# Kernel tuning notes

Hardware: AMD Instinct MI355X
Metric: run time of the kernel (lower is better)

Reference implementation:

```python
import jax, jax.numpy as jnp
import numpy as np

WIN = 9
PAD = WIN // 2
WIN_SIZE = float(WIN * WIN)
EPS = 1e-5


def _box_sum(x):
    # Equivalent to conv2d with a [1,1,9,9] ones kernel, stride 1, padding 4.
    # reduce_window with add is the efficient/clean jax form of a box filter.
    return jax.lax.reduce_window(
        x, 0.0, jax.lax.add,
        window_dimensions=(1, 1, WIN, WIN),
        window_strides=(1, 1, 1, 1),
        padding=[(0, 0), (0, 0), (PAD, PAD), (PAD, PAD)],
    )


def setup_inputs() -> dict:
    key = jax.random.key(0)
    k1, k2 = jax.random.split(key)
    shape = (16, 1, 512, 512)  # [B, C=1, H, W]
    y_true = jax.random.uniform(k1, shape, dtype=jnp.float32)
    y_pred = jax.random.uniform(k2, shape, dtype=jnp.float32)
    return {"y_true": y_true, "y_pred": y_pred}


def reference(y_true, y_pred):
    Ii, Ji = y_true, y_pred

    I_sum = _box_sum(Ii)
    J_sum = _box_sum(Ji)
    I2_sum = _box_sum(Ii * Ii)
    J2_sum = _box_sum(Ji * Ji)
    IJ_sum = _box_sum(Ii * Ji)

    u_I = I_sum / WIN_SIZE
    u_J = J_sum / WIN_SIZE

    cross = IJ_sum - u_J * I_sum - u_I * J_sum + u_I * u_J * WIN_SIZE
    cross = jnp.maximum(cross, EPS)
    I_var = I2_sum - 2.0 * u_I * I_sum + u_I * u_I * WIN_SIZE
    I_var = jnp.maximum(I_var, EPS)
    J_var = J2_sum - 2.0 * u_J * J_sum + u_J * u_J * WIN_SIZE
    J_var = jnp.maximum(J_var, EPS)

    cc = (cross * cross) / (I_var * J_var)
    return -jnp.mean(cc)
```

## Files before the change

kernel.cpp:

```cpp
#include <hip/hip_runtime.h>

#define IMG    512
#define BAND   4
#define NBLK   512
#define NPIX   (16.0 * 512.0 * 512.0)
#define EPS    1e-5f
#define INV81  (1.0f / 81.0f)

struct Rows { float4 i0, i1, j0, j1; };

__device__ __forceinline__ Rows load_rows(const float* __restrict__ Ib,
                                          const float* __restrict__ Jb,
                                          int y, int col0)
{
    Rows r;
    if (y >= 0 && y < IMG) {
        const float* rI = Ib + (size_t)y * IMG + col0;
        const float* rJ = Jb + (size_t)y * IMG + col0;
        r.i0 = *(const float4*)(rI);
        r.i1 = *(const float4*)(rI + 4);
        r.j0 = *(const float4*)(rJ);
        r.j1 = *(const float4*)(rJ + 4);
    } else {
        r.i0 = r.i1 = r.j0 = r.j1 = float4{0.f, 0.f, 0.f, 0.f};
    }
    return r;
}

#define ACC(c, xv, yv)                          \
    sI[c]  += (xv); sJ[c] += (yv);              \
    sII[c]  = fmaf((xv), (xv), sII[c]);         \
    sJJ[c]  = fmaf((yv), (yv), sJJ[c]);         \
    sIJ[c]  = fmaf((xv), (yv), sIJ[c]);

#define UPD(c, nx, ny, ox, oy)                                  \
    sI[c]  += (nx) - (ox);                                      \
    sJ[c]  += (ny) - (oy);                                      \
    sII[c]  = fmaf((nx), (nx), fmaf(-(ox), (ox), sII[c]));      \
    sJJ[c]  = fmaf((ny), (ny), fmaf(-(oy), (oy), sJJ[c]));      \
    sIJ[c]  = fmaf((nx), (ny), fmaf(-(ox), (oy), sIJ[c]));

#define ACC_ROWS(R)                              \
    ACC(0, R.i0.x, R.j0.x) ACC(1, R.i0.y, R.j0.y)\
    ACC(2, R.i0.z, R.j0.z) ACC(3, R.i0.w, R.j0.w)\
    ACC(4, R.i1.x, R.j1.x) ACC(5, R.i1.y, R.j1.y)\
    ACC(6, R.i1.z, R.j1.z) ACC(7, R.i1.w, R.j1.w)

#define UPD_ROWS(NR, OR)                                                  \
    UPD(0, NR.i0.x, NR.j0.x, OR.i0.x, OR.j0.x)                            \
    UPD(1, NR.i0.y, NR.j0.y, OR.i0.y, OR.j0.y)                            \
    UPD(2, NR.i0.z, NR.j0.z, OR.i0.z, OR.j0.z)                            \
    UPD(3, NR.i0.w, NR.j0.w, OR.i0.w, OR.j0.w)                            \
    UPD(4, NR.i1.x, NR.j1.x, OR.i1.x, OR.j1.x)                            \
    UPD(5, NR.i1.y, NR.j1.y, OR.i1.y, OR.j1.y)                            \
    UPD(6, NR.i1.z, NR.j1.z, OR.i1.z, OR.j1.z)                            \
    UPD(7, NR.i1.w, NR.j1.w, OR.i1.w, OR.j1.w)

__device__ __forceinline__ void hwin(const float s[8], int lane, float w[8])
{
    float l[4], r[4];
    #pragma unroll
    for (int i = 0; i < 4; ++i) {
        float lv = __shfl_up(s[4 + i], 1, 64);
        float rv = __shfl_down(s[i],   1, 64);
        l[i] = (lane == 0)  ? 0.f : lv;
        r[i] = (lane == 63) ? 0.f : rv;
    }
    w[0] = ((l[0] + l[1]) + (l[2] + l[3])) +
           ((s[0] + s[1]) + (s[2] + s[3])) + s[4];
    w[1] = w[0] + s[5] - l[0];
    w[2] = w[1] + s[6] - l[1];
    w[3] = w[2] + s[7] - l[2];
    w[4] = w[3] + r[0] - l[3];
    w[5] = w[4] + r[1] - s[0];
    w[6] = w[5] + r[2] - s[1];
    w[7] = w[6] + r[3] - s[2];
}

__global__ __launch_bounds__(256) void ncc_band_kernel(
    const float* __restrict__ I, const float* __restrict__ J,
    double* __restrict__ slots)
{
    const int lane = threadIdx.x & 63;
    const int wid  = threadIdx.x >> 6;
    const int sblk = (blockIdx.x & 7) * (NBLK / 8) + (blockIdx.x >> 3);
    const int band = sblk * 4 + wid;
    const int img  = band >> 7;
    const int y0   = (band & 127) * BAND;
    const int col0 = lane * 8;

    const float* Ib = I + (size_t)img * IMG * IMG;
    const float* Jb = J + (size_t)img * IMG * IMG;

    float sI[8], sJ[8], sII[8], sJJ[8], sIJ[8];
    #pragma unroll
    for (int c = 0; c < 8; ++c) { sI[c]=0.f; sJ[c]=0.f; sII[c]=0.f; sJJ[c]=0.f; sIJ[c]=0.f; }

    Rows od0 = load_rows(Ib, Jb, y0 - 4, col0);
    Rows od1 = load_rows(Ib, Jb, y0 - 3, col0);
    Rows A   = load_rows(Ib, Jb, y0 - 2, col0);
    Rows B   = load_rows(Ib, Jb, y0 - 1, col0);

    ACC_ROWS(od0)
    ACC_ROWS(od1)
    ACC_ROWS(A)  A = load_rows(Ib, Jb, y0 + 0, col0);
    ACC_ROWS(B)  B = load_rows(Ib, Jb, y0 + 1, col0);
    ACC_ROWS(A)  A = load_rows(Ib, Jb, y0 + 2, col0);
    ACC_ROWS(B)  B = load_rows(Ib, Jb, y0 + 3, col0);
    ACC_ROWS(A)  A = load_rows(Ib, Jb, y0 + 4, col0);
    ACC_ROWS(B)  B = load_rows(Ib, Jb, y0 + 5, col0);
    ACC_ROWS(A)  A = load_rows(Ib, Jb, y0 + 6, col0);

    float local = 0.0f;

    auto hpass = [&]() {
        float wI[8], wJ[8], t[8], cross[8];
        hwin(sI, lane, wI);
        hwin(sJ, lane, wJ);
        hwin(sIJ, lane, t);
        #pragma unroll
        for (int k = 0; k < 8; ++k)
            cross[k] = fmaxf(fmaf(-wI[k] * INV81, wJ[k], t[k]), EPS);
        hwin(sII, lane, t);
        #pragma unroll
        for (int k = 0; k < 8; ++k)
            wI[k] = fmaxf(fmaf(-wI[k] * INV81, wI[k], t[k]), EPS);
        hwin(sJJ, lane, t);
        #pragma unroll
        for (int k = 0; k < 8; ++k)
            wJ[k] = fmaxf(fmaf(-wJ[k] * INV81, wJ[k], t[k]), EPS);
        #pragma unroll
        for (int k = 0; k < 8; ++k)
            local += (cross[k] * cross[k]) * __builtin_amdgcn_rcpf(wI[k] * wJ[k]);
    };

    hpass();
    UPD_ROWS(B, od0)
    B = load_rows(Ib, Jb, y0 + 7, col0);
    hpass();
    UPD_ROWS(A, od1)
    A = load_rows(Ib, Jb, y0 - 2, col0);
    hpass();
    UPD_ROWS(B, A)
    hpass();

    #pragma unroll
    for (int off = 32; off > 0; off >>= 1)
        local += __shfl_down(local, off, 64);

    __shared__ float wpart[4];
    if (lane == 0) wpart[wid] = local;
    __syncthreads();
    if (threadIdx.x == 0) {
        double bsum = ((double)wpart[0] + (double)wpart[1]) +
                      ((double)wpart[2] + (double)wpart[3]);
        slots[blockIdx.x] = bsum;
    }
}

__global__ __launch_bounds__(256) void ncc_finalize_kernel(
    const double* __restrict__ slots, float* __restrict__ out)
{
    const int tid = threadIdx.x;
    double2 v = *(const double2*)(slots + 2 * tid);
    double t = v.x + v.y;
    #pragma unroll
    for (int off = 32; off > 0; off >>= 1)
        t += __shfl_down(t, off, 64);

    __shared__ double wsumd[4];
    if ((tid & 63) == 0) wsumd[tid >> 6] = t;
    __syncthreads();
    if (tid == 0)
        out[0] = (float)(-((wsumd[0] + wsumd[1]) +
                           (wsumd[2] + wsumd[3])) / NPIX);
}

extern "C" void kernel_launch(void* const* d_in, const int* in_sizes, int n_in,
                              void* d_out, int out_size, void* d_ws, size_t ws_size,
                              hipStream_t stream)
{
    const float* I = (const float*)d_in[0];
    const float* J = (const float*)d_in[1];
    float* out = (float*)d_out;
    double* slots = (double*)d_ws;

    ncc_band_kernel<<<NBLK, 256, 0, stream>>>(I, J, slots);
    ncc_finalize_kernel<<<1, 256, 0, stream>>>(slots, out);
}
```

Baseline: 16.16 us.

## Split each image row across two waves with LDS edge exchange

Each band of 4 rows is now processed by two waves, each covering half the 512 columns with 4 columns per lane instead of 8. Grid size doubles to 1024 blocks. The column-sums at the seam between the two halves are exchanged through double-buffered shared memory, with a __syncthreads before each horizontal pass. The finalize kernel now reads twice as many slots. The aim is more parallelism and lower per-thread register pressure, at the cost of block-wide barriers, LDS traffic, and row loads that are 16 bytes wide instead of 32.

New measurement: 28.02 us. 1.73x slower.

```diff
diff --git a/kernel.cpp b/kernel.cpp
--- a/kernel.cpp
+++ b/kernel.cpp
@@ -2,12 +2,12 @@
 
 #define IMG    512
 #define BAND   4
-#define NBLK   512
+#define NBLK   1024
 #define NPIX   (16.0 * 512.0 * 512.0)
 #define EPS    1e-5f
 #define INV81  (1.0f / 81.0f)
 
-struct Rows { float4 i0, i1, j0, j1; };
+struct Rows { float4 i0, j0; };
 
 __device__ __forceinline__ Rows load_rows(const float* __restrict__ Ib,
                                           const float* __restrict__ Jb,
@@ -15,14 +15,11 @@
 {
     Rows r;
     if (y >= 0 && y < IMG) {
-        const float* rI = Ib + (size_t)y * IMG + col0;
-        const float* rJ = Jb + (size_t)y * IMG + col0;
-        r.i0 = *(const float4*)(rI);
-        r.i1 = *(const float4*)(rI + 4);
-        r.j0 = *(const float4*)(rJ);
-        r.j1 = *(const float4*)(rJ + 4);
+        r.i0 = *(const float4*)(Ib + (size_t)y * IMG + col0);
+        r.j0 = *(const float4*)(Jb + (size_t)y * IMG + col0);
     } else {
-        r.i0 = r.i1 = r.j0 = r.j1 = float4{0.f, 0.f, 0.f, 0.f};
+        r.i0 = float4{0.f, 0.f, 0.f, 0.f};
+        r.j0 = float4{0.f, 0.f, 0.f, 0.f};
     }
     return r;
 }
@@ -40,109 +37,137 @@
     sJJ[c]  = fmaf((ny), (ny), fmaf(-(oy), (oy), sJJ[c]));      \
     sIJ[c]  = fmaf((nx), (ny), fmaf(-(ox), (oy), sIJ[c]));
 
-#define ACC_ROWS(R)                              \
+#define ACC4(R)                                  \
     ACC(0, R.i0.x, R.j0.x) ACC(1, R.i0.y, R.j0.y)\
-    ACC(2, R.i0.z, R.j0.z) ACC(3, R.i0.w, R.j0.w)\
-    ACC(4, R.i1.x, R.j1.x) ACC(5, R.i1.y, R.j1.y)\
-    ACC(6, R.i1.z, R.j1.z) ACC(7, R.i1.w, R.j1.w)
-
-#define UPD_ROWS(NR, OR)                                                  \
+    ACC(2, R.i0.z, R.j0.z) ACC(3, R.i0.w, R.j0.w)
+
+#define UPD4(NR, OR)                                                      \
     UPD(0, NR.i0.x, NR.j0.x, OR.i0.x, OR.j0.x)                            \
     UPD(1, NR.i0.y, NR.j0.y, OR.i0.y, OR.j0.y)                            \
     UPD(2, NR.i0.z, NR.j0.z, OR.i0.z, OR.j0.z)                            \
-    UPD(3, NR.i0.w, NR.j0.w, OR.i0.w, OR.j0.w)                            \
-    UPD(4, NR.i1.x, NR.j1.x, OR.i1.x, OR.j1.x)                            \
-    UPD(5, NR.i1.y, NR.j1.y, OR.i1.y, OR.j1.y)                            \
-    UPD(6, NR.i1.z, NR.j1.z, OR.i1.z, OR.j1.z)                            \
-    UPD(7, NR.i1.w, NR.j1.w, OR.i1.w, OR.j1.w)
-
-__device__ __forceinline__ void hwin(const float s[8], int lane, float w[8])
+    UPD(3, NR.i0.w, NR.j0.w, OR.i0.w, OR.j0.w)
+
+__device__ __forceinline__ void hwin4(const float s[4], const float* lSrc,
+                                      const float* rSrc, int lane, float w[4])
 {
     float l[4], r[4];
     #pragma unroll
     for (int i = 0; i < 4; ++i) {
-        float lv = __shfl_up(s[4 + i], 1, 64);
-        float rv = __shfl_down(s[i],   1, 64);
-        l[i] = (lane == 0)  ? 0.f : lv;
-        r[i] = (lane == 63) ? 0.f : rv;
+        float lv = __shfl_up(s[i], 1, 64);
+        float rv = __shfl_down(s[i], 1, 64);
+        l[i] = (lane == 0)  ? lSrc[i] : lv;
+        r[i] = (lane == 63) ? rSrc[i] : rv;
     }
     w[0] = ((l[0] + l[1]) + (l[2] + l[3])) +
-           ((s[0] + s[1]) + (s[2] + s[3])) + s[4];
-    w[1] = w[0] + s[5] - l[0];
-    w[2] = w[1] + s[6] - l[1];
-    w[3] = w[2] + s[7] - l[2];
-    w[4] = w[3] + r[0] - l[3];
-    w[5] = w[4] + r[1] - s[0];
-    w[6] = w[5] + r[2] - s[1];
-    w[7] = w[6] + r[3] - s[2];
+           ((s[0] + s[1]) + (s[2] + s[3])) + r[0];
+    w[1] = w[0] + r[1] - l[0];
+    w[2] = w[1] + r[2] - l[1];
+    w[3] = w[2] + r[3] - l[2];
 }
 
 __global__ __launch_bounds__(256) void ncc_band_kernel(
     const float* __restrict__ I, const float* __restrict__ J,
     double* __restrict__ slots)
 {
-    const int lane = threadIdx.x & 63;
-    const int wid  = threadIdx.x >> 6;
-    const int sblk = (blockIdx.x & 7) * (NBLK / 8) + (blockIdx.x >> 3);
-    const int band = sblk * 4 + wid;
-    const int img  = band >> 7;
-    const int y0   = (band & 127) * BAND;
-    const int col0 = lane * 8;
+    const int lane  = threadIdx.x & 63;
+    const int wid   = threadIdx.x >> 6;
+    const int sblk  = (blockIdx.x & 7) * (NBLK / 8) + (blockIdx.x >> 3);
+    const int band  = sblk * 2 + (wid >> 1);
+    const int cside = wid & 1;
+    const int img   = band >> 7;
+    const int y0    = (band & 127) * BAND;
+    const int col0  = cside * 256 + lane * 4;
 
     const float* Ib = I + (size_t)img * IMG * IMG;
     const float* Jb = J + (size_t)img * IMG * IMG;
 
-    float sI[8], sJ[8], sII[8], sJJ[8], sIJ[8];
-    #pragma unroll
-    for (int c = 0; c < 8; ++c) { sI[c]=0.f; sJ[c]=0.f; sII[c]=0.f; sJJ[c]=0.f; sIJ[c]=0.f; }
+    __shared__ float eL[2][4][20];
+    __shared__ float eR[2][4][20];
+    if (threadIdx.x < 160) {
+        (&eL[0][0][0])[threadIdx.x] = 0.f;
+        (&eR[0][0][0])[threadIdx.x] = 0.f;
+    }
+    __syncthreads();
+
+    float sI[4], sJ[4], sII[4], sJJ[4], sIJ[4];
+    #pragma unroll
+    for (int c = 0; c < 4; ++c) { sI[c]=0.f; sJ[c]=0.f; sII[c]=0.f; sJJ[c]=0.f; sIJ[c]=0.f; }
 
     Rows od0 = load_rows(Ib, Jb, y0 - 4, col0);
     Rows od1 = load_rows(Ib, Jb, y0 - 3, col0);
     Rows A   = load_rows(Ib, Jb, y0 - 2, col0);
     Rows B   = load_rows(Ib, Jb, y0 - 1, col0);
 
-    ACC_ROWS(od0)
-    ACC_ROWS(od1)
-    ACC_ROWS(A)  A = load_rows(Ib, Jb, y0 + 0, col0);
-    ACC_ROWS(B)  B = load_rows(Ib, Jb, y0 + 1, col0);
-    ACC_ROWS(A)  A = load_rows(Ib, Jb, y0 + 2, col0);
-    ACC_ROWS(B)  B = load_rows(Ib, Jb, y0 + 3, col0);
-    ACC_ROWS(A)  A = load_rows(Ib, Jb, y0 + 4, col0);
-    ACC_ROWS(B)  B = load_rows(Ib, Jb, y0 + 5, col0);
-    ACC_ROWS(A)  A = load_rows(Ib, Jb, y0 + 6, col0);
+    ACC4(od0)
+    ACC4(od1)
+    ACC4(A)  A = load_rows(Ib, Jb, y0 + 0, col0);
+    ACC4(B)  B = load_rows(Ib, Jb, y0 + 1, col0);
+    ACC4(A)  A = load_rows(Ib, Jb, y0 + 2, col0);
+    ACC4(B)  B = load_rows(Ib, Jb, y0 + 3, col0);
+    ACC4(A)  A = load_rows(Ib, Jb, y0 + 4, col0);
+    ACC4(B)  B = load_rows(Ib, Jb, y0 + 5, col0);
+    ACC4(A)  A = load_rows(Ib, Jb, y0 + 6, col0);
 
     float local = 0.0f;
 
-    auto hpass = [&]() {
-        float wI[8], wJ[8], t[8], cross[8];
-        hwin(sI, lane, wI);
-        hwin(sJ, lane, wJ);
-        hwin(sIJ, lane, t);
-        #pragma unroll
-        for (int k = 0; k < 8; ++k)
+    auto edge_write = [&](int buf) {
+        if (cside == 0) {
+            if (lane == 63) {
+                float* d = &eL[buf][wid + 1][0];
+                *(float4*)(d +  0) = float4{sI[0],  sI[1],  sI[2],  sI[3]};
+                *(float4*)(d +  4) = float4{sJ[0],  sJ[1],  sJ[2],  sJ[3]};
+                *(float4*)(d +  8) = float4{sII[0], sII[1], sII[2], sII[3]};
+                *(float4*)(d + 12) = float4{sJJ[0], sJJ[1], sJJ[2], sJJ[3]};
+                *(float4*)(d + 16) = float4{sIJ[0], sIJ[1], sIJ[2], sIJ[3]};
+            }
+        } else {
+            if (lane == 0) {
+                float* d = &eR[buf][wid - 1][0];
+                *(float4*)(d +  0) = float4{sI[0],  sI[1],  sI[2],  sI[3]};
+                *(float4*)(d +  4) = float4{sJ[0],  sJ[1],  sJ[2],  sJ[3]};
+                *(float4*)(d +  8) = float4{sII[0], sII[1], sII[2], sII[3]};
+                *(float4*)(d + 12) = float4{sJJ[0], sJJ[1], sJJ[2], sJJ[3]};
+                *(float4*)(d + 16) = float4{sIJ[0], sIJ[1], sIJ[2], sIJ[3]};
+            }
+        }
+    };
+
+    auto hpass = [&](int buf) {
+        const float* Lb = &eL[buf][wid][0];
+        const float* Rb = &eR[buf][wid][0];
+        float wI[4], wJ[4], t[4], cross[4];
+        hwin4(sI,  Lb + 0,  Rb + 0,  lane, wI);
+        hwin4(sJ,  Lb + 4,  Rb + 4,  lane, wJ);
+        hwin4(sIJ, Lb + 16, Rb + 16, lane, t);
+        #pragma unroll
+        for (int k = 0; k < 4; ++k)
             cross[k] = fmaxf(fmaf(-wI[k] * INV81, wJ[k], t[k]), EPS);
-        hwin(sII, lane, t);
-        #pragma unroll
-        for (int k = 0; k < 8; ++k)
+        hwin4(sII, Lb + 8,  Rb + 8,  lane, t);
+        #pragma unroll
+        for (int k = 0; k < 4; ++k)
             wI[k] = fmaxf(fmaf(-wI[k] * INV81, wI[k], t[k]), EPS);
-        hwin(sJJ, lane, t);
-        #pragma unroll
-        for (int k = 0; k < 8; ++k)
+        hwin4(sJJ, Lb + 12, Rb + 12, lane, t);
+        #pragma unroll
+        for (int k = 0; k < 4; ++k)
             wJ[k] = fmaxf(fmaf(-wJ[k] * INV81, wJ[k], t[k]), EPS);
         #pragma unroll
-        for (int k = 0; k < 8; ++k)
+        for (int k = 0; k < 4; ++k)
             local += (cross[k] * cross[k]) * __builtin_amdgcn_rcpf(wI[k] * wJ[k]);
     };
 
-    hpass();
-    UPD_ROWS(B, od0)
+    edge_write(0); __syncthreads();
+    hpass(0);
+    UPD4(B, od0)
     B = load_rows(Ib, Jb, y0 + 7, col0);
-    hpass();
-    UPD_ROWS(A, od1)
+    edge_write(1); __syncthreads();
+    hpass(1);
+    UPD4(A, od1)
     A = load_rows(Ib, Jb, y0 - 2, col0);
-    hpass();
-    UPD_ROWS(B, A)
-    hpass();
+    edge_write(0); __syncthreads();
+    hpass(0);
+    UPD4(B, A)
+    edge_write(1); __syncthreads();
+    hpass(1);
 
     #pragma unroll
     for (int off = 32; off > 0; off >>= 1)
@@ -162,8 +187,9 @@
     const double* __restrict__ slots, float* __restrict__ out)
 {
     const int tid = threadIdx.x;
-    double2 v = *(const double2*)(slots + 2 * tid);
-    double t = v.x + v.y;
+    double2 v0 = *(const double2*)(slots + 2 * tid);
+    double2 v1 = *(const double2*)(slots + 512 + 2 * tid);
+    double t = (v0.x + v0.y) + (v1.x + v1.y);
     #pragma unroll
     for (int off = 32; off > 0; off >>= 1)
         t += __shfl_down(t, off, 64);
```
